# Optimization experiments

Measured on AMD Instinct MI355X. Metric: run time of the kernel, lower is better.

Reference implementation:

```python
import jax, jax.numpy as jnp
import numpy as np

N, DEG, F, H, O, B = 100000, 16, 128, 128, 128, 8192


def setup_inputs() -> dict:
    key = jax.random.key(0)
    k1, k2, k3, k4, k5 = jax.random.split(key, 5)
    features = jax.random.normal(k1, (N, F), dtype=jnp.float32)
    w1 = jax.random.normal(k2, (2 * F, H), dtype=jnp.float32)
    w2 = jax.random.normal(k3, (2 * H, O), dtype=jnp.float32)
    neighbor_idx = jax.random.randint(k4, (N, DEG), 0, N, dtype=jnp.int32)
    nodes = jax.random.randint(k5, (B,), 0, N, dtype=jnp.int32)
    return {"features": features, "w1": w1, "w2": w2,
            "neighbor_idx": neighbor_idx, "nodes": nodes}


def reference(features, w1, w2, neighbor_idx, nodes):
    # Layer 1 (computed for all nodes, vectorized): mean-aggregate neighbor
    # raw features, concat with self features, project with w1.
    neigh_feat = features[neighbor_idx]                 # [N, DEG, F] gather
    agg1 = neigh_feat.mean(axis=1)                      # [N, F]
    h1 = jnp.concatenate([features, agg1], axis=-1) @ w1  # [N, H]

    # Layer 2 (batch nodes): mean-aggregate neighbor layer-1 embeddings,
    # concat with self layer-1 embedding, project with w2.
    h1_self = h1[nodes]                                 # [B, H]
    h1_neigh = h1[neighbor_idx[nodes]].mean(axis=1)     # [B, H]
    out = jnp.concatenate([h1_self, h1_neigh], axis=-1) @ w2  # [B, O]
    return out
```

## Files before the change

### kernel.cpp

```cpp
#include <hip/hip_runtime.h>


#define N_NODES 100000
#define DEG     16
#define FDIM    128
#define HDIM    128
#define B_NODES 8192

typedef __attribute__((ext_vector_type(8))) short bf16x8;
typedef __attribute__((ext_vector_type(8))) unsigned short u16x8;
typedef __attribute__((ext_vector_type(4))) float f32x4;
typedef __attribute__((ext_vector_type(2))) float f32x2;

static __device__ __forceinline__ unsigned short f2bf(float f) {
    union { float f; unsigned u; } v; v.f = f;
    unsigned r = v.u + 0x7fff + ((v.u >> 16) & 1);
    return (unsigned short)(r >> 16);
}
static __device__ __forceinline__ float bf2f(unsigned short b) {
    union { unsigned u; float f; } v; v.u = ((unsigned)b) << 16;
    return v.f;
}

__global__ __launch_bounds__(256)
void prep(const float* __restrict__ feat, const float* __restrict__ w1,
          const float* __restrict__ w2, unsigned short* __restrict__ fb,
          unsigned char* __restrict__ f8,
          unsigned short* __restrict__ w1T, unsigned short* __restrict__ w2T) {
    if (blockIdx.x < 6250) {
        long e = ((long)blockIdx.x * 256 + threadIdx.x) * 8;
        float4 v0 = *(const float4*)(feat + e);
        float4 v1 = *(const float4*)(feat + e + 4);
        u16x8 ob;
        ob[0] = f2bf(v0.x); ob[1] = f2bf(v0.y); ob[2] = f2bf(v0.z); ob[3] = f2bf(v0.w);
        ob[4] = f2bf(v1.x); ob[5] = f2bf(v1.y); ob[6] = f2bf(v1.z); ob[7] = f2bf(v1.w);
        *(u16x8*)(fb + e) = ob;
        int p0 = 0, p1 = 0;
        p0 = __builtin_amdgcn_cvt_pk_fp8_f32(v0.x, v0.y, p0, false);
        p0 = __builtin_amdgcn_cvt_pk_fp8_f32(v0.z, v0.w, p0, true);
        p1 = __builtin_amdgcn_cvt_pk_fp8_f32(v1.x, v1.y, p1, false);
        p1 = __builtin_amdgcn_cvt_pk_fp8_f32(v1.z, v1.w, p1, true);
        uint2 o8; o8.x = (unsigned)p0; o8.y = (unsigned)p1;
        *(uint2*)(f8 + e) = o8;
    } else {
        int bid = blockIdx.x - 6250;
        const float* w = (bid < 8) ? w1 : w2;
        unsigned short* wT = (bid < 8) ? w1T : w2T;
        int kb = (bid & 7) * 32;
        int n = threadIdx.x & 127, dk = threadIdx.x >> 7;
#pragma unroll
        for (int i = 0; i < 16; ++i) {
            int k = kb + dk * 16 + i;
            wT[n * 256 + k] = f2bf(w[k * 128 + n]);
        }
    }
}

__global__ __launch_bounds__(64)
void k1_agg(const unsigned char* __restrict__ f8, const int* __restrict__ nbr,
            unsigned short* __restrict__ agg) {
    __shared__ unsigned char L[16][1024];
    const int lane = threadIdx.x;
    const int node = blockIdx.x * 8 + (lane >> 3);
    const int sub = lane & 7;
    const int* idx = nbr + node * DEG;
    int4 i0 = *(const int4*)(idx);
    int4 i1 = *(const int4*)(idx + 4);
    int4 i2 = *(const int4*)(idx + 8);
    int4 i3 = *(const int4*)(idx + 12);
    const int id[16] = {i0.x, i0.y, i0.z, i0.w, i1.x, i1.y, i1.z, i1.w,
                        i2.x, i2.y, i2.z, i2.w, i3.x, i3.y, i3.z, i3.w};
#pragma unroll
    for (int d = 0; d < DEG; ++d) {
        const unsigned char* src = f8 + (long)id[d] * 128 + sub * 16;
        __builtin_amdgcn_global_load_lds(
            (const __attribute__((address_space(1))) unsigned int*)src,
            (__attribute__((address_space(3))) unsigned int*)(&L[d][lane * 16]),
            16, 0, 0);
    }
    asm volatile("s_waitcnt vmcnt(0)" ::: "memory");

    f32x2 s2[8];
#pragma unroll
    for (int j = 0; j < 8; ++j) s2[j] = (f32x2){0.f, 0.f};
#pragma unroll
    for (int d = 0; d < DEG; ++d) {
        uint4 v = *(const uint4*)(&L[d][lane * 16]);
        s2[0] += __builtin_amdgcn_cvt_pk_f32_fp8((int)v.x, false);
        s2[1] += __builtin_amdgcn_cvt_pk_f32_fp8((int)v.x, true);
        s2[2] += __builtin_amdgcn_cvt_pk_f32_fp8((int)v.y, false);
        s2[3] += __builtin_amdgcn_cvt_pk_f32_fp8((int)v.y, true);
        s2[4] += __builtin_amdgcn_cvt_pk_f32_fp8((int)v.z, false);
        s2[5] += __builtin_amdgcn_cvt_pk_f32_fp8((int)v.z, true);
        s2[6] += __builtin_amdgcn_cvt_pk_f32_fp8((int)v.w, false);
        s2[7] += __builtin_amdgcn_cvt_pk_f32_fp8((int)v.w, true);
    }
    u16x8 o0, o1;
#pragma unroll
    for (int j = 0; j < 8; ++j) {
        o0[j] = f2bf(s2[j >> 1][j & 1] * 0.0625f);
        o1[j] = f2bf(s2[4 + (j >> 1)][j & 1] * 0.0625f);
    }
    unsigned short* dst = agg + (long)node * 128 + sub * 16;
    *(u16x8*)dst = o0;
    *(u16x8*)(dst + 8) = o1;
}

#define STAGE(KC, BUF)                                                                        \
    do {                                                                                      \
        const unsigned short* s0_ = ((KC) < 4) ? (fb + (KC) * 32) : (agg + ((KC) - 4) * 32);  \
        _Pragma("unroll")                                                                     \
        for (int j_ = 0; j_ < 2; ++j_) {                                                      \
            long grow_ = row0 + (t >> 2) + j_ * 64;                                           \
            const unsigned short* ga_ = s0_ + grow_ * 128 + (t & 3) * 8;                      \
            __builtin_amdgcn_global_load_lds(                                                 \
                (const __attribute__((address_space(1))) unsigned int*)ga_,                   \
                (__attribute__((address_space(3))) unsigned int*)                             \
                    (&AsS[(BUF) * 4096 + wave * 512 + j_ * 2048 + lane * 8]), 16, 0, 0);      \
            const unsigned short* gw_ = w1T + ((t >> 2) + j_ * 64) * 256 + (KC) * 32 + (t & 3) * 8; \
            __builtin_amdgcn_global_load_lds(                                                 \
                (const __attribute__((address_space(1))) unsigned int*)gw_,                   \
                (__attribute__((address_space(3))) unsigned int*)                             \
                    (&WsS[(BUF) * 4096 + wave * 512 + j_ * 2048 + lane * 8]), 16, 0, 0);      \
        }                                                                                     \
    } while (0)

__global__ __launch_bounds__(256, 4)
void g1(const unsigned short* __restrict__ fb, const unsigned short* __restrict__ agg,
        const unsigned short* __restrict__ w1T, unsigned short* __restrict__ h1) {
    __shared__ unsigned short AsS[2 * 4096];
    __shared__ unsigned short WsS[2 * 4096];
    const int t = threadIdx.x, wave = t >> 6, lane = t & 63;
    const int m16 = lane & 15, quad = lane >> 4;
    const long row0 = (long)blockIdx.x * 128;

    f32x4 acc[2][8] = {};
    STAGE(0, 0);
#pragma unroll
    for (int kc = 0; kc < 8; ++kc) {
        __syncthreads();
        if (kc < 7) {
            switch (kc + 1) {
                case 1: STAGE(1, 1); break;
                case 2: STAGE(2, 0); break;
                case 3: STAGE(3, 1); break;
                case 4: STAGE(4, 0); break;
                case 5: STAGE(5, 1); break;
                case 6: STAGE(6, 0); break;
                case 7: STAGE(7, 1); break;
            }
        }
        const unsigned short* Ab = &AsS[(kc & 1) * 4096];
        const unsigned short* Wb = &WsS[(kc & 1) * 4096];
        bf16x8 a0 = *(const bf16x8*)(Ab + (wave * 32 + m16) * 32 + quad * 8);
        bf16x8 a1 = *(const bf16x8*)(Ab + (wave * 32 + 16 + m16) * 32 + quad * 8);
#pragma unroll
        for (int nt = 0; nt < 8; ++nt) {
            bf16x8 bv = *(const bf16x8*)(Wb + (nt * 16 + m16) * 32 + quad * 8);
            acc[0][nt] = __builtin_amdgcn_mfma_f32_16x16x32_bf16(a0, bv, acc[0][nt], 0, 0, 0);
            acc[1][nt] = __builtin_amdgcn_mfma_f32_16x16x32_bf16(a1, bv, acc[1][nt], 0, 0, 0);
        }
    }

#pragma unroll
    for (int mt = 0; mt < 2; ++mt)
#pragma unroll
        for (int reg = 0; reg < 4; ++reg) {
            long grow = row0 + wave * 32 + mt * 16 + quad * 4 + reg;
            if (grow >= N_NODES) continue;
#pragma unroll
            for (int nt = 0; nt < 8; ++nt)
                h1[grow * HDIM + nt * 16 + m16] = f2bf(acc[mt][nt][reg]);
        }
}

__global__ __launch_bounds__(256)
void g2_fused(const unsigned short* __restrict__ h1, const unsigned short* __restrict__ w2T,
              const int* __restrict__ nbr, const int* __restrict__ nodes,
              float* __restrict__ out) {
    __shared__ unsigned short X2[64][264];
    const int t = threadIdx.x, wave = t >> 6, lane = t & 63;
    const int m16 = lane & 15, quad = lane >> 4;
    const int b0 = blockIdx.x * 64;
    const int colb = m16 * 8;

    for (int g = 0; g < 4; ++g) {
        int Ln = wave * 16 + g * 4 + quad;
        int node = nodes[b0 + Ln];
        *(u16x8*)(&X2[Ln][colb]) = *(const u16x8*)(h1 + node * HDIM + colb);
        const int* idx = nbr + node * DEG;
        float s[8] = {0.f, 0.f, 0.f, 0.f, 0.f, 0.f, 0.f, 0.f};
#pragma unroll
        for (int d = 0; d < DEG; ++d) {
            int nb = idx[d];
            u16x8 v = *(const u16x8*)(h1 + nb * HDIM + colb);
#pragma unroll
            for (int j = 0; j < 8; ++j) s[j] += bf2f(v[j]);
        }
        u16x8 o;
#pragma unroll
        for (int j = 0; j < 8; ++j) o[j] = f2bf(s[j] * 0.0625f);
        *(u16x8*)(&X2[Ln][128 + colb]) = o;
    }
    __syncthreads();

    f32x4 acc[8] = {};
#pragma unroll
    for (int kc = 0; kc < 8; ++kc) {
        bf16x8 a = *(const bf16x8*)(&X2[wave * 16 + m16][kc * 32 + quad * 8]);
#pragma unroll
        for (int nt = 0; nt < 8; ++nt) {
            bf16x8 b = *(const bf16x8*)(w2T + (nt * 16 + m16) * 256 + kc * 32 + quad * 8);
            acc[nt] = __builtin_amdgcn_mfma_f32_16x16x32_bf16(a, b, acc[nt], 0, 0, 0);
        }
    }

#pragma unroll
    for (int nt = 0; nt < 8; ++nt)
#pragma unroll
        for (int reg = 0; reg < 4; ++reg) {
            int row = b0 + wave * 16 + quad * 4 + reg;
            out[row * 128 + nt * 16 + m16] = acc[nt][reg];
        }
}

extern "C" void kernel_launch(void* const* d_in, const int* in_sizes, int n_in,
                              void* d_out, int out_size, void* d_ws, size_t ws_size,
                              hipStream_t stream) {
    const float* feat  = (const float*)d_in[0];
    const float* w1    = (const float*)d_in[1];
    const float* w2    = (const float*)d_in[2];
    const int*   nbr   = (const int*)d_in[3];
    const int*   nodes = (const int*)d_in[4];
    float* out = (float*)d_out;

    char* ws = (char*)d_ws;
    unsigned short* fb  = (unsigned short*)ws;
    unsigned char*  f8  = (unsigned char*)(ws + 25600000);
    unsigned short* agg = (unsigned short*)(ws + 38400000);
    unsigned short* h1  = (unsigned short*)(ws + 64000000);
    unsigned short* w1T = (unsigned short*)(ws + 89600000);
    unsigned short* w2T = (unsigned short*)(ws + 89665536);

    prep<<<6266, 256, 0, stream>>>(feat, w1, w2, fb, f8, w1T, w2T);
    k1_agg<<<12500, 64, 0, stream>>>(f8, nbr, agg);
    g1<<<(N_NODES + 127) / 128, 256, 0, stream>>>(fb, agg, w1T, h1);
    g2_fused<<<B_NODES / 64, 256, 0, stream>>>(h1, w2T, nbr, nodes, out);
}
```

Before: 164.6 us.

## Drop LDS staging in aggregation and GEMM kernels, use direct register loads

k1_agg now runs 256-thread blocks and gathers fp8 neighbor rows straight into registers in two batches of eight, with no LDS staging. g1 loses its double-buffered LDS pipeline and __syncthreads; each wave reads its A rows and the w1T fragments directly from global memory. g2_fused is split into 64-thread single-wave blocks with a smaller LDS tile and no barrier. The aim is to cut LDS traffic, barrier stalls and waitcnt serialization and to raise occupancy, at the cost of redundant global reads of w1T per wave and less coalesced A loads in g1.

```diff
diff --git a/kernel.cpp b/kernel.cpp
--- a/kernel.cpp
+++ b/kernel.cpp
@@ -56,13 +56,12 @@
     }
 }
 
-__global__ __launch_bounds__(64)
+__global__ __launch_bounds__(256, 4)
 void k1_agg(const unsigned char* __restrict__ f8, const int* __restrict__ nbr,
             unsigned short* __restrict__ agg) {
-    __shared__ unsigned char L[16][1024];
-    const int lane = threadIdx.x;
-    const int node = blockIdx.x * 8 + (lane >> 3);
-    const int sub = lane & 7;
+    const int t = threadIdx.x;
+    const int node = blockIdx.x * 32 + (t >> 3);
+    const int sub = t & 7;
     const int* idx = nbr + node * DEG;
     int4 i0 = *(const int4*)(idx);
     int4 i1 = *(const int4*)(idx + 4);
@@ -70,31 +69,30 @@
     int4 i3 = *(const int4*)(idx + 12);
     const int id[16] = {i0.x, i0.y, i0.z, i0.w, i1.x, i1.y, i1.z, i1.w,
                         i2.x, i2.y, i2.z, i2.w, i3.x, i3.y, i3.z, i3.w};
-#pragma unroll
-    for (int d = 0; d < DEG; ++d) {
-        const unsigned char* src = f8 + (long)id[d] * 128 + sub * 16;
-        __builtin_amdgcn_global_load_lds(
-            (const __attribute__((address_space(1))) unsigned int*)src,
-            (__attribute__((address_space(3))) unsigned int*)(&L[d][lane * 16]),
-            16, 0, 0);
-    }
-    asm volatile("s_waitcnt vmcnt(0)" ::: "memory");
 
     f32x2 s2[8];
 #pragma unroll
     for (int j = 0; j < 8; ++j) s2[j] = (f32x2){0.f, 0.f};
-#pragma unroll
-    for (int d = 0; d < DEG; ++d) {
-        uint4 v = *(const uint4*)(&L[d][lane * 16]);
-        s2[0] += __builtin_amdgcn_cvt_pk_f32_fp8((int)v.x, false);
-        s2[1] += __builtin_amdgcn_cvt_pk_f32_fp8((int)v.x, true);
-        s2[2] += __builtin_amdgcn_cvt_pk_f32_fp8((int)v.y, false);
-        s2[3] += __builtin_amdgcn_cvt_pk_f32_fp8((int)v.y, true);
-        s2[4] += __builtin_amdgcn_cvt_pk_f32_fp8((int)v.z, false);
-        s2[5] += __builtin_amdgcn_cvt_pk_f32_fp8((int)v.z, true);
-        s2[6] += __builtin_amdgcn_cvt_pk_f32_fp8((int)v.w, false);
-        s2[7] += __builtin_amdgcn_cvt_pk_f32_fp8((int)v.w, true);
-    }
+
+    uint4 v[8];
+#pragma unroll
+    for (int h = 0; h < 2; ++h) {
+#pragma unroll
+        for (int d = 0; d < 8; ++d)
+            v[d] = *(const uint4*)(f8 + (long)id[h * 8 + d] * 128 + sub * 16);
+#pragma unroll
+        for (int d = 0; d < 8; ++d) {
+            s2[0] += __builtin_amdgcn_cvt_pk_f32_fp8((int)v[d].x, false);
+            s2[1] += __builtin_amdgcn_cvt_pk_f32_fp8((int)v[d].x, true);
+            s2[2] += __builtin_amdgcn_cvt_pk_f32_fp8((int)v[d].y, false);
+            s2[3] += __builtin_amdgcn_cvt_pk_f32_fp8((int)v[d].y, true);
+            s2[4] += __builtin_amdgcn_cvt_pk_f32_fp8((int)v[d].z, false);
+            s2[5] += __builtin_amdgcn_cvt_pk_f32_fp8((int)v[d].z, true);
+            s2[6] += __builtin_amdgcn_cvt_pk_f32_fp8((int)v[d].w, false);
+            s2[7] += __builtin_amdgcn_cvt_pk_f32_fp8((int)v[d].w, true);
+        }
+    }
+
     u16x8 o0, o1;
 #pragma unroll
     for (int j = 0; j < 8; ++j) {
@@ -106,57 +104,22 @@
     *(u16x8*)(dst + 8) = o1;
 }
 
-#define STAGE(KC, BUF)                                                                        \
-    do {                                                                                      \
-        const unsigned short* s0_ = ((KC) < 4) ? (fb + (KC) * 32) : (agg + ((KC) - 4) * 32);  \
-        _Pragma("unroll")                                                                     \
-        for (int j_ = 0; j_ < 2; ++j_) {                                                      \
-            long grow_ = row0 + (t >> 2) + j_ * 64;                                           \
-            const unsigned short* ga_ = s0_ + grow_ * 128 + (t & 3) * 8;                      \
-            __builtin_amdgcn_global_load_lds(                                                 \
-                (const __attribute__((address_space(1))) unsigned int*)ga_,                   \
-                (__attribute__((address_space(3))) unsigned int*)                             \
-                    (&AsS[(BUF) * 4096 + wave * 512 + j_ * 2048 + lane * 8]), 16, 0, 0);      \
-            const unsigned short* gw_ = w1T + ((t >> 2) + j_ * 64) * 256 + (KC) * 32 + (t & 3) * 8; \
-            __builtin_amdgcn_global_load_lds(                                                 \
-                (const __attribute__((address_space(1))) unsigned int*)gw_,                   \
-                (__attribute__((address_space(3))) unsigned int*)                             \
-                    (&WsS[(BUF) * 4096 + wave * 512 + j_ * 2048 + lane * 8]), 16, 0, 0);      \
-        }                                                                                     \
-    } while (0)
-
-__global__ __launch_bounds__(256, 4)
+__global__ __launch_bounds__(256, 3)
 void g1(const unsigned short* __restrict__ fb, const unsigned short* __restrict__ agg,
         const unsigned short* __restrict__ w1T, unsigned short* __restrict__ h1) {
-    __shared__ unsigned short AsS[2 * 4096];
-    __shared__ unsigned short WsS[2 * 4096];
     const int t = threadIdx.x, wave = t >> 6, lane = t & 63;
     const int m16 = lane & 15, quad = lane >> 4;
-    const long row0 = (long)blockIdx.x * 128;
+    const long row0 = (long)blockIdx.x * 128 + wave * 32;
 
     f32x4 acc[2][8] = {};
-    STAGE(0, 0);
 #pragma unroll
     for (int kc = 0; kc < 8; ++kc) {
-        __syncthreads();
-        if (kc < 7) {
-            switch (kc + 1) {
-                case 1: STAGE(1, 1); break;
-                case 2: STAGE(2, 0); break;
-                case 3: STAGE(3, 1); break;
-                case 4: STAGE(4, 0); break;
-                case 5: STAGE(5, 1); break;
-                case 6: STAGE(6, 0); break;
-                case 7: STAGE(7, 1); break;
-            }
-        }
-        const unsigned short* Ab = &AsS[(kc & 1) * 4096];
-        const unsigned short* Wb = &WsS[(kc & 1) * 4096];
-        bf16x8 a0 = *(const bf16x8*)(Ab + (wave * 32 + m16) * 32 + quad * 8);
-        bf16x8 a1 = *(const bf16x8*)(Ab + (wave * 32 + 16 + m16) * 32 + quad * 8);
+        const unsigned short* As = (kc < 4) ? (fb + kc * 32) : (agg + (kc - 4) * 32);
+        bf16x8 a0 = *(const bf16x8*)(As + (row0 + m16) * 128 + quad * 8);
+        bf16x8 a1 = *(const bf16x8*)(As + (row0 + 16 + m16) * 128 + quad * 8);
 #pragma unroll
         for (int nt = 0; nt < 8; ++nt) {
-            bf16x8 bv = *(const bf16x8*)(Wb + (nt * 16 + m16) * 32 + quad * 8);
+            bf16x8 bv = *(const bf16x8*)(w1T + (nt * 16 + m16) * 256 + kc * 32 + quad * 8);
             acc[0][nt] = __builtin_amdgcn_mfma_f32_16x16x32_bf16(a0, bv, acc[0][nt], 0, 0, 0);
             acc[1][nt] = __builtin_amdgcn_mfma_f32_16x16x32_bf16(a1, bv, acc[1][nt], 0, 0, 0);
         }
@@ -166,7 +129,7 @@
     for (int mt = 0; mt < 2; ++mt)
 #pragma unroll
         for (int reg = 0; reg < 4; ++reg) {
-            long grow = row0 + wave * 32 + mt * 16 + quad * 4 + reg;
+            long grow = row0 + mt * 16 + quad * 4 + reg;
             if (grow >= N_NODES) continue;
 #pragma unroll
             for (int nt = 0; nt < 8; ++nt)
@@ -174,26 +137,27 @@
         }
 }
 
-__global__ __launch_bounds__(256)
+__global__ __launch_bounds__(64)
 void g2_fused(const unsigned short* __restrict__ h1, const unsigned short* __restrict__ w2T,
               const int* __restrict__ nbr, const int* __restrict__ nodes,
               float* __restrict__ out) {
-    __shared__ unsigned short X2[64][264];
-    const int t = threadIdx.x, wave = t >> 6, lane = t & 63;
+    __shared__ unsigned short X2[16][264];
+    const int lane = threadIdx.x;
     const int m16 = lane & 15, quad = lane >> 4;
-    const int b0 = blockIdx.x * 64;
+    const int b0 = blockIdx.x * 16;
     const int colb = m16 * 8;
 
+#pragma unroll
     for (int g = 0; g < 4; ++g) {
-        int Ln = wave * 16 + g * 4 + quad;
+        int Ln = g * 4 + quad;
         int node = nodes[b0 + Ln];
-        *(u16x8*)(&X2[Ln][colb]) = *(const u16x8*)(h1 + node * HDIM + colb);
+        *(u16x8*)(&X2[Ln][colb]) = *(const u16x8*)(h1 + (long)node * HDIM + colb);
         const int* idx = nbr + node * DEG;
         float s[8] = {0.f, 0.f, 0.f, 0.f, 0.f, 0.f, 0.f, 0.f};
 #pragma unroll
         for (int d = 0; d < DEG; ++d) {
             int nb = idx[d];
-            u16x8 v = *(const u16x8*)(h1 + nb * HDIM + colb);
+            u16x8 v = *(const u16x8*)(h1 + (long)nb * HDIM + colb);
 #pragma unroll
             for (int j = 0; j < 8; ++j) s[j] += bf2f(v[j]);
         }
@@ -202,12 +166,11 @@
         for (int j = 0; j < 8; ++j) o[j] = f2bf(s[j] * 0.0625f);
         *(u16x8*)(&X2[Ln][128 + colb]) = o;
     }
-    __syncthreads();
 
     f32x4 acc[8] = {};
 #pragma unroll
     for (int kc = 0; kc < 8; ++kc) {
-        bf16x8 a = *(const bf16x8*)(&X2[wave * 16 + m16][kc * 32 + quad * 8]);
+        bf16x8 a = *(const bf16x8*)(&X2[m16][kc * 32 + quad * 8]);
 #pragma unroll
         for (int nt = 0; nt < 8; ++nt) {
             bf16x8 b = *(const bf16x8*)(w2T + (nt * 16 + m16) * 256 + kc * 32 + quad * 8);
@@ -219,8 +182,8 @@
     for (int nt = 0; nt < 8; ++nt)
 #pragma unroll
         for (int reg = 0; reg < 4; ++reg) {
-            int row = b0 + wave * 16 + quad * 4 + reg;
-            out[row * 128 + nt * 16 + m16] = acc[nt][reg];
+            int row = b0 + quad * 4 + reg;
+            out[(long)row * 128 + nt * 16 + m16] = acc[nt][reg];
         }
 }
 
@@ -243,7 +206,7 @@
     unsigned short* w2T = (unsigned short*)(ws + 89665536);
 
     prep<<<6266, 256, 0, stream>>>(feat, w1, w2, fb, f8, w1T, w2T);
-    k1_agg<<<12500, 64, 0, stream>>>(f8, nbr, agg);
+    k1_agg<<<3125, 256, 0, stream>>>(f8, nbr, agg);
     g1<<<(N_NODES + 127) / 128, 256, 0, stream>>>(fb, agg, w1T, h1);
-    g2_fused<<<B_NODES / 64, 256, 0, stream>>>(h1, w2T, nbr, nodes, out);
-}
+    g2_fused<<<B_NODES / 64 * 4, 64, 0, stream>>>(h1, w2T, nbr, nodes, out);
+}
```

Result: slower. 191.8 us (+16.5%).

## Load g1 A fragments directly to registers and stage full W1 in LDS once

Applied to the files above, without the earlier changes.

The g1 GEMM no longer double-buffers A and W tiles through LDS with a barrier on every k-step. Each wave loads all of its A fragments for the full K=256 straight from global memory into registers. The whole transposed w1 (64KB) is copied into LDS once in MFMA fragment order, followed by a single barrier. This removes the per-step syncs and the A round-trip through LDS, but raises register and LDS use, so occupancy is lowered to 2 blocks per CU.

```diff
diff --git a/kernel.cpp b/kernel.cpp
--- a/kernel.cpp
+++ b/kernel.cpp
@@ -106,59 +106,46 @@
     *(u16x8*)(dst + 8) = o1;
 }
 
-#define STAGE(KC, BUF)                                                                        \
-    do {                                                                                      \
-        const unsigned short* s0_ = ((KC) < 4) ? (fb + (KC) * 32) : (agg + ((KC) - 4) * 32);  \
-        _Pragma("unroll")                                                                     \
-        for (int j_ = 0; j_ < 2; ++j_) {                                                      \
-            long grow_ = row0 + (t >> 2) + j_ * 64;                                           \
-            const unsigned short* ga_ = s0_ + grow_ * 128 + (t & 3) * 8;                      \
-            __builtin_amdgcn_global_load_lds(                                                 \
-                (const __attribute__((address_space(1))) unsigned int*)ga_,                   \
-                (__attribute__((address_space(3))) unsigned int*)                             \
-                    (&AsS[(BUF) * 4096 + wave * 512 + j_ * 2048 + lane * 8]), 16, 0, 0);      \
-            const unsigned short* gw_ = w1T + ((t >> 2) + j_ * 64) * 256 + (KC) * 32 + (t & 3) * 8; \
-            __builtin_amdgcn_global_load_lds(                                                 \
-                (const __attribute__((address_space(1))) unsigned int*)gw_,                   \
-                (__attribute__((address_space(3))) unsigned int*)                             \
-                    (&WsS[(BUF) * 4096 + wave * 512 + j_ * 2048 + lane * 8]), 16, 0, 0);      \
-        }                                                                                     \
-    } while (0)
-
-__global__ __launch_bounds__(256, 4)
+__global__ __launch_bounds__(256, 2)
 void g1(const unsigned short* __restrict__ fb, const unsigned short* __restrict__ agg,
         const unsigned short* __restrict__ w1T, unsigned short* __restrict__ h1) {
-    __shared__ unsigned short AsS[2 * 4096];
-    __shared__ unsigned short WsS[2 * 4096];
+    __shared__ unsigned short Wlds[64 * 512];
     const int t = threadIdx.x, wave = t >> 6, lane = t & 63;
     const int m16 = lane & 15, quad = lane >> 4;
-    const long row0 = (long)blockIdx.x * 128;
+    const long row0 = (long)blockIdx.x * 128 + wave * 32;
+
+    bf16x8 a[8][2];
+#pragma unroll
+    for (int kc = 0; kc < 8; ++kc) {
+        const unsigned short* As = (kc < 4) ? (fb + kc * 32) : (agg + (kc - 4) * 32);
+        a[kc][0] = *(const bf16x8*)(As + (row0 + m16) * 128 + quad * 8);
+        a[kc][1] = *(const bf16x8*)(As + (row0 + 16 + m16) * 128 + quad * 8);
+    }
+
+#pragma unroll
+    for (int i = 0; i < 16; ++i) {
+        int o16 = i * 256 + t;
+        int chunk = o16 >> 6;
+        int kc = chunk >> 3, nt = chunk & 7;
+        int n = nt * 16 + (lane & 15);
+        int k0 = kc * 32 + (lane >> 4) * 8;
+        const unsigned short* src = w1T + n * 256 + k0;
+        __builtin_amdgcn_global_load_lds(
+            (const __attribute__((address_space(1))) unsigned int*)src,
+            (__attribute__((address_space(3))) unsigned int*)
+                (((char*)Wlds) + (long)o16 * 16),
+            16, 0, 0);
+    }
+    __syncthreads();
 
     f32x4 acc[2][8] = {};
-    STAGE(0, 0);
 #pragma unroll
     for (int kc = 0; kc < 8; ++kc) {
-        __syncthreads();
-        if (kc < 7) {
-            switch (kc + 1) {
-                case 1: STAGE(1, 1); break;
-                case 2: STAGE(2, 0); break;
-                case 3: STAGE(3, 1); break;
-                case 4: STAGE(4, 0); break;
-                case 5: STAGE(5, 1); break;
-                case 6: STAGE(6, 0); break;
-                case 7: STAGE(7, 1); break;
-            }
-        }
-        const unsigned short* Ab = &AsS[(kc & 1) * 4096];
-        const unsigned short* Wb = &WsS[(kc & 1) * 4096];
-        bf16x8 a0 = *(const bf16x8*)(Ab + (wave * 32 + m16) * 32 + quad * 8);
-        bf16x8 a1 = *(const bf16x8*)(Ab + (wave * 32 + 16 + m16) * 32 + quad * 8);
 #pragma unroll
         for (int nt = 0; nt < 8; ++nt) {
-            bf16x8 bv = *(const bf16x8*)(Wb + (nt * 16 + m16) * 32 + quad * 8);
-            acc[0][nt] = __builtin_amdgcn_mfma_f32_16x16x32_bf16(a0, bv, acc[0][nt], 0, 0, 0);
-            acc[1][nt] = __builtin_amdgcn_mfma_f32_16x16x32_bf16(a1, bv, acc[1][nt], 0, 0, 0);
+            bf16x8 bv = *(const bf16x8*)(Wlds + (kc * 8 + nt) * 512 + lane * 8);
+            acc[0][nt] = __builtin_amdgcn_mfma_f32_16x16x32_bf16(a[kc][0], bv, acc[0][nt], 0, 0, 0);
+            acc[1][nt] = __builtin_amdgcn_mfma_f32_16x16x32_bf16(a[kc][1], bv, acc[1][nt], 0, 0, 0);
         }
     }
 
@@ -166,7 +153,7 @@
     for (int mt = 0; mt < 2; ++mt)
 #pragma unroll
         for (int reg = 0; reg < 4; ++reg) {
-            long grow = row0 + wave * 32 + mt * 16 + quad * 4 + reg;
+            long grow = row0 + mt * 16 + quad * 4 + reg;
             if (grow >= N_NODES) continue;
 #pragma unroll
             for (int nt = 0; nt < 8; ++nt)
```

Result: slower. 170.8 us (+3.8%).

## Double-buffer the layer-1 neighbor gather and batch all layer-2 gather loads

Applied to the files above, without the earlier changes.

The layer-1 aggregation now streams its 16 neighbor rows through two 4-row LDS buffers. Partial `s_waitcnt` counts let fp8 conversion and accumulation overlap with the loads still in flight, and LDS per block drops from 16 KB to 8 KB. The layer-2 fused kernel now loads the neighbor indices as int4 vectors and issues all 16 neighbor-row loads up front via inline asm. It then sums the first half while the second half is still arriving. The aim is to hide gather latency and raise the number of loads in flight. The cost is hand-managed wait counts and asm, which are brittle if the compiler reorders or adds memory operations.

```diff
diff --git a/kernel.cpp b/kernel.cpp
--- a/kernel.cpp
+++ b/kernel.cpp
@@ -59,7 +59,7 @@
 __global__ __launch_bounds__(64)
 void k1_agg(const unsigned char* __restrict__ f8, const int* __restrict__ nbr,
             unsigned short* __restrict__ agg) {
-    __shared__ unsigned char L[16][1024];
+    __shared__ unsigned char L[8][1024];
     const int lane = threadIdx.x;
     const int node = blockIdx.x * 8 + (lane >> 3);
     const int sub = lane & 7;
@@ -70,31 +70,54 @@
     int4 i3 = *(const int4*)(idx + 12);
     const int id[16] = {i0.x, i0.y, i0.z, i0.w, i1.x, i1.y, i1.z, i1.w,
                         i2.x, i2.y, i2.z, i2.w, i3.x, i3.y, i3.z, i3.w};
-#pragma unroll
-    for (int d = 0; d < DEG; ++d) {
-        const unsigned char* src = f8 + (long)id[d] * 128 + sub * 16;
-        __builtin_amdgcn_global_load_lds(
-            (const __attribute__((address_space(1))) unsigned int*)src,
-            (__attribute__((address_space(3))) unsigned int*)(&L[d][lane * 16]),
-            16, 0, 0);
-    }
+
+#define K1_ISSUE(Q, B)                                                          \
+    _Pragma("unroll")                                                           \
+    for (int j_ = 0; j_ < 4; ++j_) {                                            \
+        const unsigned char* src_ = f8 + (long)id[(Q) * 4 + j_] * 128 + sub * 16; \
+        __builtin_amdgcn_global_load_lds(                                       \
+            (const __attribute__((address_space(1))) unsigned int*)src_,        \
+            (__attribute__((address_space(3))) unsigned int*)                   \
+                (&L[(B) * 4 + j_][lane * 16]), 16, 0, 0);                       \
+    }
+
+    f32x2 s2[8];
+#pragma unroll
+    for (int j = 0; j < 8; ++j) s2[j] = (f32x2){0.f, 0.f};
+
+#define K1_CONV(B)                                                              \
+    _Pragma("unroll")                                                           \
+    for (int j_ = 0; j_ < 4; ++j_) {                                            \
+        uint4 v = *(const uint4*)(&L[(B) * 4 + j_][lane * 16]);                 \
+        s2[0] += __builtin_amdgcn_cvt_pk_f32_fp8((int)v.x, false);              \
+        s2[1] += __builtin_amdgcn_cvt_pk_f32_fp8((int)v.x, true);               \
+        s2[2] += __builtin_amdgcn_cvt_pk_f32_fp8((int)v.y, false);              \
+        s2[3] += __builtin_amdgcn_cvt_pk_f32_fp8((int)v.y, true);               \
+        s2[4] += __builtin_amdgcn_cvt_pk_f32_fp8((int)v.z, false);              \
+        s2[5] += __builtin_amdgcn_cvt_pk_f32_fp8((int)v.z, true);               \
+        s2[6] += __builtin_amdgcn_cvt_pk_f32_fp8((int)v.w, false);              \
+        s2[7] += __builtin_amdgcn_cvt_pk_f32_fp8((int)v.w, true);               \
+    }
+
+    K1_ISSUE(0, 0);
+    K1_ISSUE(1, 1);
+    asm volatile("s_waitcnt vmcnt(4)" ::: "memory");
+    __builtin_amdgcn_sched_barrier(0);
+    K1_CONV(0);
+    __builtin_amdgcn_sched_barrier(0);
+    K1_ISSUE(2, 0);
+    asm volatile("s_waitcnt vmcnt(4)" ::: "memory");
+    __builtin_amdgcn_sched_barrier(0);
+    K1_CONV(1);
+    __builtin_amdgcn_sched_barrier(0);
+    K1_ISSUE(3, 1);
+    asm volatile("s_waitcnt vmcnt(4)" ::: "memory");
+    __builtin_amdgcn_sched_barrier(0);
+    K1_CONV(0);
     asm volatile("s_waitcnt vmcnt(0)" ::: "memory");
-
-    f32x2 s2[8];
-#pragma unroll
-    for (int j = 0; j < 8; ++j) s2[j] = (f32x2){0.f, 0.f};
-#pragma unroll
-    for (int d = 0; d < DEG; ++d) {
-        uint4 v = *(const uint4*)(&L[d][lane * 16]);
-        s2[0] += __builtin_amdgcn_cvt_pk_f32_fp8((int)v.x, false);
-        s2[1] += __builtin_amdgcn_cvt_pk_f32_fp8((int)v.x, true);
-        s2[2] += __builtin_amdgcn_cvt_pk_f32_fp8((int)v.y, false);
-        s2[3] += __builtin_amdgcn_cvt_pk_f32_fp8((int)v.y, true);
-        s2[4] += __builtin_amdgcn_cvt_pk_f32_fp8((int)v.z, false);
-        s2[5] += __builtin_amdgcn_cvt_pk_f32_fp8((int)v.z, true);
-        s2[6] += __builtin_amdgcn_cvt_pk_f32_fp8((int)v.w, false);
-        s2[7] += __builtin_amdgcn_cvt_pk_f32_fp8((int)v.w, true);
-    }
+    __builtin_amdgcn_sched_barrier(0);
+    K1_CONV(1);
+
     u16x8 o0, o1;
 #pragma unroll
     for (int j = 0; j < 8; ++j) {
@@ -187,16 +210,46 @@
     for (int g = 0; g < 4; ++g) {
         int Ln = wave * 16 + g * 4 + quad;
         int node = nodes[b0 + Ln];
-        *(u16x8*)(&X2[Ln][colb]) = *(const u16x8*)(h1 + node * HDIM + colb);
+        *(u16x8*)(&X2[Ln][colb]) = *(const u16x8*)(h1 + (long)node * HDIM + colb);
         const int* idx = nbr + node * DEG;
+        int4 i0 = *(const int4*)(idx);
+        int4 i1 = *(const int4*)(idx + 4);
+        int4 i2 = *(const int4*)(idx + 8);
+        int4 i3 = *(const int4*)(idx + 12);
+        const int id[16] = {i0.x, i0.y, i0.z, i0.w, i1.x, i1.y, i1.z, i1.w,
+                            i2.x, i2.y, i2.z, i2.w, i3.x, i3.y, i3.z, i3.w};
+
+        uint4 v0, v1, v2, v3, v4, v5, v6, v7, v8, v9, v10, v11, v12, v13, v14, v15;
+#define G2_LOAD(K)                                                               \
+        {                                                                        \
+            unsigned long long a_ =                                              \
+                (unsigned long long)(h1 + (long)id[K] * HDIM + colb);            \
+            asm volatile("global_load_dwordx4 %0, %1, off"                       \
+                         : "=v"(v##K) : "v"(a_) : "memory");                     \
+        }
+        G2_LOAD(0)  G2_LOAD(1)  G2_LOAD(2)  G2_LOAD(3)
+        G2_LOAD(4)  G2_LOAD(5)  G2_LOAD(6)  G2_LOAD(7)
+        G2_LOAD(8)  G2_LOAD(9)  G2_LOAD(10) G2_LOAD(11)
+        G2_LOAD(12) G2_LOAD(13) G2_LOAD(14) G2_LOAD(15)
+#undef G2_LOAD
+
         float s[8] = {0.f, 0.f, 0.f, 0.f, 0.f, 0.f, 0.f, 0.f};
-#pragma unroll
-        for (int d = 0; d < DEG; ++d) {
-            int nb = idx[d];
-            u16x8 v = *(const u16x8*)(h1 + nb * HDIM + colb);
-#pragma unroll
-            for (int j = 0; j < 8; ++j) s[j] += bf2f(v[j]);
-        }
+        asm volatile("s_waitcnt vmcnt(8)" ::: "memory");
+        __builtin_amdgcn_sched_barrier(0);
+#define G2_SUM(K)                                                                \
+        {                                                                        \
+            u16x8 w_ = __builtin_bit_cast(u16x8, v##K);                          \
+            _Pragma("unroll")                                                    \
+            for (int j = 0; j < 8; ++j) s[j] += bf2f(w_[j]);                     \
+        }
+        G2_SUM(0) G2_SUM(1) G2_SUM(2) G2_SUM(3)
+        G2_SUM(4) G2_SUM(5) G2_SUM(6) G2_SUM(7)
+        asm volatile("s_waitcnt vmcnt(0)" ::: "memory");
+        __builtin_amdgcn_sched_barrier(0);
+        G2_SUM(8)  G2_SUM(9)  G2_SUM(10) G2_SUM(11)
+        G2_SUM(12) G2_SUM(13) G2_SUM(14) G2_SUM(15)
+#undef G2_SUM
+
         u16x8 o;
 #pragma unroll
         for (int j = 0; j < 8; ++j) o[j] = f2bf(s[j] * 0.0625f);
@@ -220,7 +273,7 @@
 #pragma unroll
         for (int reg = 0; reg < 4; ++reg) {
             int row = b0 + wave * 16 + quad * 4 + reg;
-            out[row * 128 + nt * 16 + m16] = acc[nt][reg];
+            out[(long)row * 128 + nt * 16 + m16] = acc[nt][reg];
         }
 }
 
```

Result: no change. 165.8 us (+0.7%).
